# Kernel optimization log

Hardware: AMD Instinct MI355X
Metric: run time of the kernel (lower is better)

The kernel has to match this reference:

```python
import jax, jax.numpy as jnp
import numpy as np

X_MIN, X_MAX = -3.0, 3.0
EPS = 1e-08


def setup_inputs() -> dict:
    key = jax.random.key(0)
    k1, k2, k3 = jax.random.split(key, 3)
    B, D_in, D_out, K = 8192, 512, 128, 16
    x = jax.random.normal(k1, (B, D_in), dtype=jnp.float32)
    # trunc_normal_(std=0.02) approximated by scaled normal
    weights = jax.random.normal(k2, (D_out, D_in, K), dtype=jnp.float32) * 0.02
    # xavier_uniform for skip
    limit = float(np.sqrt(6.0 / (D_in + D_out)))
    skip_w = jax.random.uniform(k3, (D_out, D_in), dtype=jnp.float32,
                                minval=-limit, maxval=limit)
    bias = jnp.zeros((D_out,), dtype=jnp.float32)
    return {"x": x, "weights": weights, "skip_w": skip_w, "bias": bias}


def reference(x, weights, skip_w, bias):
    # x: (B, D_in); weights: (D_out, D_in, K); skip_w: (D_out, D_in); bias: (D_out,)
    K = weights.shape[-1]
    t = jnp.clip((x - X_MIN) / (X_MAX - X_MIN + EPS), 0.0, 1.0)
    pos = t * (K - 1)
    idx0 = jnp.floor(pos).astype(jnp.int32)
    idx1 = jnp.minimum(idx0 + 1, K - 1)
    frac = jnp.clip(pos - idx0.astype(pos.dtype), 0.0, 1.0)
    # Hat-basis coefficients per (b, i): avoids materializing (B, D_out, D_in)
    oh0 = jax.nn.one_hot(idx0, K, dtype=x.dtype)  # (B, D_in, K)
    oh1 = jax.nn.one_hot(idx1, K, dtype=x.dtype)
    c = oh0 * (1.0 - frac)[..., None] + oh1 * frac[..., None]  # (B, D_in, K)
    # y[b,o] = sum_i (1-frac)*w[o,i,idx0] + frac*w[o,i,idx1]
    y = jnp.einsum('bik,oik->bo', c, weights)
    y = y + bias + x @ skip_w.T
    return y
```

## Files before the change

kernel.cpp:

```cpp
#include <hip/hip_runtime.h>

typedef __attribute__((ext_vector_type(8))) short short8;
typedef __attribute__((ext_vector_type(4))) float f32x4;

#define DIN 512
#define DOUT 128
#define KK 16
#define BTOT 8192
#define KAUG (DIN * KK + DIN)
#define NCHUNK_TOT (KAUG / 128)
#define NSPL 4
#define CPB (NCHUNK_TOT / NSPL)
#define BM 64
#define CHUNK_BYTES 32768
#define CBASE 32768
#define LDS_BYTES 49152

__device__ static inline unsigned short f2bf(float x) {
  unsigned u = __builtin_bit_cast(unsigned, x);
  return (unsigned short)((u + 0x7FFFu + ((u >> 16) & 1u)) >> 16);
}

__device__ static inline void llds16(const char* g, char* l) {
  __builtin_amdgcn_global_load_lds(
      (const __attribute__((address_space(1))) unsigned int*)g,
      (__attribute__((address_space(3))) unsigned int*)l, 16, 0, 0);
}

__global__ __launch_bounds__(256) void build_wpp(const float* __restrict__ w,
                                                 const float* __restrict__ sk,
                                                 unsigned short* __restrict__ wpp) {
  const int gi = blockIdx.x * 256 + threadIdx.x;
  const int g = gi >> 11;
  const int rem = gi & 2047;
  const int o = rem >> 4;
  const int kcs = rem & 15;
  const int kc = kcs ^ (o & 15);
  const int kglob = g * 128 + kc * 8;
  const float* src = (kglob < 8192) ? (w + (size_t)o * 8192 + kglob)
                                    : (sk + (size_t)o * 512 + (kglob - 8192));
  const float4 v0 = ((const float4*)src)[0];
  const float4 v1 = ((const float4*)src)[1];
  uint4 pk;
  pk.x = f2bf(v0.x) | ((unsigned)f2bf(v0.y) << 16);
  pk.y = f2bf(v0.z) | ((unsigned)f2bf(v0.w) << 16);
  pk.z = f2bf(v1.x) | ((unsigned)f2bf(v1.y) << 16);
  pk.w = f2bf(v1.z) | ((unsigned)f2bf(v1.w) << 16);
  ((uint4*)wpp)[gi] = pk;
}

__global__ __launch_bounds__(256, 2) void kan_mfma(const float* __restrict__ x,
                                                   const unsigned short* __restrict__ wpp,
                                                   const float* __restrict__ bias,
                                                   float* __restrict__ out) {
  __shared__ __align__(16) char smem[LDS_BYTES];
  const int tid = threadIdx.x;
  const int bt = blockIdx.x >> 2;
  const int sp = blockIdx.x & 3;
  const int b0 = bt * BM;
  const int wid = tid >> 6, lane = tid & 63;
  const int lr = lane & 15, lq = lane >> 4;
  const int wm = wid & 1, wn = wid >> 1;

  f32x4 acc[2][4] = {};

  for (int c = 0; c < CPB; ++c) {
    const int g = sp * CPB + c;
    __syncthreads();

    {
      const char* gsrc = ((const char*)wpp) + (size_t)g * CHUNK_BYTES + wid * 8192 + lane * 16;
      char* ldst = smem + wid * 8192;
#pragma unroll
      for (int it = 0; it < 8; ++it)
        llds16(gsrc + it * 1024, ldst + it * 1024);
    }

    if (g < 64) {
      const int ibase = g * 8;
#pragma unroll
      for (int hh = 0; hh < 2; ++hh) {
        const int p = tid + hh * 256;
        const int bl = p >> 3, il = p & 7;
        const float xv = x[(size_t)(b0 + bl) * DIN + ibase + il];
        float t = fminf(fmaxf((xv + 3.0f) * (1.0f / 6.0f), 0.0f), 1.0f);
        const float pos = t * 15.0f;
        int i0 = (int)pos;
        i0 = i0 > 14 ? 14 : i0;
        const float f = pos - (float)i0;
        char* row = smem + CBASE + bl * 256;
        const int swz = bl & 15;
        char* g0 = row + (((il * 2) ^ swz) << 4);
        char* g1 = row + (((il * 2 + 1) ^ swz) << 4);
        *(uint4*)g0 = make_uint4(0, 0, 0, 0);
        *(uint4*)g1 = make_uint4(0, 0, 0, 0);
        const unsigned short h0 = f2bf(1.0f - f);
        const unsigned short h1 = f2bf(f);
        const int i1 = i0 + 1;
        *(unsigned short*)(((i0 & 8) ? g1 : g0) + (i0 & 7) * 2) = h0;
        *(unsigned short*)(((i1 & 8) ? g1 : g0) + (i1 & 7) * 2) = h1;
      }
    } else {
      const int ioff = (g - 64) * 128;
      const int bl = tid >> 2, q = tid & 3;
      const float* xr = x + (size_t)(b0 + bl) * DIN + ioff;
      char* row = smem + CBASE + bl * 256;
      const int swz = bl & 15;
#pragma unroll
      for (int gg = 0; gg < 4; ++gg) {
        const int kc = q * 4 + gg;
        const float4 v0 = ((const float4*)(xr + kc * 8))[0];
        const float4 v1 = ((const float4*)(xr + kc * 8))[1];
        uint4 pk;
        pk.x = f2bf(v0.x) | ((unsigned)f2bf(v0.y) << 16);
        pk.y = f2bf(v0.z) | ((unsigned)f2bf(v0.w) << 16);
        pk.z = f2bf(v1.x) | ((unsigned)f2bf(v1.y) << 16);
        pk.w = f2bf(v1.z) | ((unsigned)f2bf(v1.w) << 16);
        *(uint4*)(row + ((kc ^ swz) << 4)) = pk;
      }
    }
    __syncthreads();

#pragma unroll
    for (int ks = 0; ks < 4; ++ks) {
      const int swq = ((ks * 4 + lq) ^ lr) << 4;
      short8 af[2], bfr[4];
#pragma unroll
      for (int mt = 0; mt < 2; ++mt) {
        const int m = wm * 32 + mt * 16 + lr;
        af[mt] = *(const short8*)(smem + CBASE + m * 256 + swq);
      }
#pragma unroll
      for (int nt = 0; nt < 4; ++nt) {
        const int o = wn * 64 + nt * 16 + lr;
        bfr[nt] = *(const short8*)(smem + o * 256 + swq);
      }
#pragma unroll
      for (int mt = 0; mt < 2; ++mt)
#pragma unroll
        for (int nt = 0; nt < 4; ++nt)
          acc[mt][nt] = __builtin_amdgcn_mfma_f32_16x16x32_bf16(af[mt], bfr[nt], acc[mt][nt], 0, 0, 0);
    }
  }

#pragma unroll
  for (int nt = 0; nt < 4; ++nt) {
    const int col = wn * 64 + nt * 16 + lr;
    const float bv = (sp == 0) ? bias[col] : 0.0f;
#pragma unroll
    for (int mt = 0; mt < 2; ++mt) {
      const int rowb = b0 + wm * 32 + mt * 16 + lq * 4;
#pragma unroll
      for (int r = 0; r < 4; ++r)
        atomicAdd(out + (size_t)(rowb + r) * DOUT + col, acc[mt][nt][r] + bv);
    }
  }
}

__global__ void kan_naive(const float* __restrict__ x, const float* __restrict__ w,
                          const float* __restrict__ skw, const float* __restrict__ bias,
                          float* __restrict__ out) {
  const int b = blockIdx.x;
  const int o = threadIdx.x;
  float acc = bias[o];
  for (int i = 0; i < DIN; ++i) {
    float xv = x[(size_t)b * DIN + i];
    float t = fminf(fmaxf((xv + 3.0f) * (1.0f / 6.0f), 0.0f), 1.0f);
    float p = t * 15.0f;
    float fi = floorf(p);
    int i0 = (int)fi;
    int i1 = (i0 < 15) ? i0 + 1 : 15;
    float f = p - fi;
    const float* wr = &w[((size_t)o * DIN + i) * KK];
    acc += (1.0f - f) * wr[i0] + f * wr[i1] + xv * skw[(size_t)o * DIN + i];
  }
  out[(size_t)b * DOUT + o] = acc;
}

extern "C" void kernel_launch(void* const* d_in, const int* in_sizes, int n_in,
                              void* d_out, int out_size, void* d_ws, size_t ws_size,
                              hipStream_t stream) {
  const float* x    = (const float*)d_in[0];
  const float* w    = (const float*)d_in[1];
  const float* skw  = (const float*)d_in[2];
  const float* bias = (const float*)d_in[3];
  float* out = (float*)d_out;

  const size_t need = (size_t)NCHUNK_TOT * CHUNK_BYTES;
  if (ws_size < need) {
    kan_naive<<<BTOT, DOUT, 0, stream>>>(x, w, skw, bias, out);
    return;
  }

  unsigned short* wpp = (unsigned short*)d_ws;

  hipMemsetAsync(d_out, 0, (size_t)out_size * sizeof(float), stream);
  build_wpp<<<NCHUNK_TOT * 2048 / 256, 256, 0, stream>>>(w, skw, wpp);
  kan_mfma<<<(BTOT / BM) * NSPL, 256, 0, stream>>>(x, wpp, bias, out);
}
```

Before: 108.7 us.

## Double-buffer weight chunks and build spline A-fragments directly in registers

Weight chunks are now double-buffered in LDS, with the next chunk's async global-to-LDS load issued before the current chunk's MFMAs. This leaves one barrier per chunk instead of two. The hat-basis and skip A-operands are built per lane straight into MFMA fragment registers from prefetched x values, so the LDS staging, zeroing and readback of the coefficient tile go away. The cost is 64KB of LDS per block, which may limit occupancy at launch bounds 2, plus redundant spline computation across the waves that share rows.

```diff
diff --git a/kernel.cpp b/kernel.cpp
--- a/kernel.cpp
+++ b/kernel.cpp
@@ -2,6 +2,7 @@
 
 typedef __attribute__((ext_vector_type(8))) short short8;
 typedef __attribute__((ext_vector_type(4))) float f32x4;
+typedef __attribute__((ext_vector_type(4))) unsigned uint4v;
 
 #define DIN 512
 #define DOUT 128
@@ -13,8 +14,7 @@
 #define CPB (NCHUNK_TOT / NSPL)
 #define BM 64
 #define CHUNK_BYTES 32768
-#define CBASE 32768
-#define LDS_BYTES 49152
+#define LDS_BYTES 65536
 
 __device__ static inline unsigned short f2bf(float x) {
   unsigned u = __builtin_bit_cast(unsigned, x);
@@ -25,6 +25,34 @@
   __builtin_amdgcn_global_load_lds(
       (const __attribute__((address_space(1))) unsigned int*)g,
       (__attribute__((address_space(3))) unsigned int*)l, 16, 0, 0);
+}
+
+__device__ static inline short8 spline_granule(float xv, int half) {
+  float t = fminf(fmaxf((xv + 3.0f) * (1.0f / 6.0f), 0.0f), 1.0f);
+  float pos = t * 15.0f;
+  int i0 = (int)pos;
+  i0 = i0 > 14 ? 14 : i0;
+  float f = pos - (float)i0;
+  unsigned h0 = f2bf(1.0f - f);
+  unsigned h1 = f2bf(f);
+  unsigned long long P = (unsigned long long)(h0 | ((unsigned)h1 << 16));
+  const int j0 = i0 - (half << 3);
+  const unsigned ju = (unsigned)j0;
+  unsigned long long Pl = P << ((j0 & 3) << 4);
+  unsigned long long spill = P >> 16;
+  unsigned long long lo = (ju < 4u) ? Pl : ((j0 == -1) ? spill : 0ULL);
+  unsigned long long hi = ((ju - 4u) < 4u) ? Pl : ((j0 == 3) ? spill : 0ULL);
+  struct U { unsigned long long a, b; } u{lo, hi};
+  return __builtin_bit_cast(short8, u);
+}
+
+__device__ static inline short8 pack8(float4 a, float4 b) {
+  uint4v p;
+  p.x = f2bf(a.x) | ((unsigned)f2bf(a.y) << 16);
+  p.y = f2bf(a.z) | ((unsigned)f2bf(a.w) << 16);
+  p.z = f2bf(b.x) | ((unsigned)f2bf(b.y) << 16);
+  p.w = f2bf(b.z) | ((unsigned)f2bf(b.w) << 16);
+  return __builtin_bit_cast(short8, p);
 }
 
 __global__ __launch_bounds__(256) void build_wpp(const float* __restrict__ w,
@@ -61,86 +89,98 @@
   const int wid = tid >> 6, lane = tid & 63;
   const int lr = lane & 15, lq = lane >> 4;
   const int wm = wid & 1, wn = wid >> 1;
+  const int g0 = sp * CPB;
 
   f32x4 acc[2][4] = {};
 
-  for (int c = 0; c < CPB; ++c) {
-    const int g = sp * CPB + c;
-    __syncthreads();
-
-    {
-      const char* gsrc = ((const char*)wpp) + (size_t)g * CHUNK_BYTES + wid * 8192 + lane * 16;
-      char* ldst = smem + wid * 8192;
-#pragma unroll
-      for (int it = 0; it < 8; ++it)
-        llds16(gsrc + it * 1024, ldst + it * 1024);
-    }
-
+  const float* xr0 = x + (size_t)(b0 + wm * 32 + lr) * DIN;
+  const float* xr1 = xr0 + 16 * DIN;
+
+  {
+    const char* gsrc = (const char*)wpp + (size_t)g0 * CHUNK_BYTES + wid * 8192 + lane * 16;
+    char* ldst = smem + wid * 8192;
+#pragma unroll
+    for (int it = 0; it < 8; ++it) llds16(gsrc + it * 1024, ldst + it * 1024);
+  }
+  float xvA[2][4], xvB[2][4];
+  {
+    const int ib = g0 * 8 + (lq >> 1);
+#pragma unroll
+    for (int ks = 0; ks < 4; ++ks) {
+      xvA[0][ks] = xr0[ib + ks * 2];
+      xvA[1][ks] = xr1[ib + ks * 2];
+    }
+  }
+  __syncthreads();
+
+  auto chunk_body = [&](int c, int cb, float (&xcur)[2][4], float (&xnxt)[2][4]) {
+    const int g = g0 + c;
+    const bool haveNext = (c + 1 < CPB);
+
+    float4 r0[4][2], r1[4][2];
+    if (g >= 64) {
+      const int koff = (g - 64) * 128 + lq * 8;
+#pragma unroll
+      for (int ks = 0; ks < 4; ++ks) {
+        r0[ks][0] = ((const float4*)(xr0 + koff + ks * 32))[0];
+        r0[ks][1] = ((const float4*)(xr0 + koff + ks * 32))[1];
+        r1[ks][0] = ((const float4*)(xr1 + koff + ks * 32))[0];
+        r1[ks][1] = ((const float4*)(xr1 + koff + ks * 32))[1];
+      }
+    }
+
+    if (haveNext) {
+      const char* gsrc = (const char*)wpp + (size_t)(g + 1) * CHUNK_BYTES + wid * 8192 + lane * 16;
+      char* ldst = smem + (cb ^ 32768) + wid * 8192;
+#pragma unroll
+      for (int it = 0; it < 8; ++it) llds16(gsrc + it * 1024, ldst + it * 1024);
+    }
+    if (haveNext && (g + 1 < 64)) {
+      const int ib = (g + 1) * 8 + (lq >> 1);
+#pragma unroll
+      for (int ks = 0; ks < 4; ++ks) {
+        xnxt[0][ks] = xr0[ib + ks * 2];
+        xnxt[1][ks] = xr1[ib + ks * 2];
+      }
+    }
+
+    short8 af[2][4];
     if (g < 64) {
-      const int ibase = g * 8;
-#pragma unroll
-      for (int hh = 0; hh < 2; ++hh) {
-        const int p = tid + hh * 256;
-        const int bl = p >> 3, il = p & 7;
-        const float xv = x[(size_t)(b0 + bl) * DIN + ibase + il];
-        float t = fminf(fmaxf((xv + 3.0f) * (1.0f / 6.0f), 0.0f), 1.0f);
-        const float pos = t * 15.0f;
-        int i0 = (int)pos;
-        i0 = i0 > 14 ? 14 : i0;
-        const float f = pos - (float)i0;
-        char* row = smem + CBASE + bl * 256;
-        const int swz = bl & 15;
-        char* g0 = row + (((il * 2) ^ swz) << 4);
-        char* g1 = row + (((il * 2 + 1) ^ swz) << 4);
-        *(uint4*)g0 = make_uint4(0, 0, 0, 0);
-        *(uint4*)g1 = make_uint4(0, 0, 0, 0);
-        const unsigned short h0 = f2bf(1.0f - f);
-        const unsigned short h1 = f2bf(f);
-        const int i1 = i0 + 1;
-        *(unsigned short*)(((i0 & 8) ? g1 : g0) + (i0 & 7) * 2) = h0;
-        *(unsigned short*)(((i1 & 8) ? g1 : g0) + (i1 & 7) * 2) = h1;
+      const int half = lq & 1;
+#pragma unroll
+      for (int ks = 0; ks < 4; ++ks) {
+        af[0][ks] = spline_granule(xcur[0][ks], half);
+        af[1][ks] = spline_granule(xcur[1][ks], half);
       }
     } else {
-      const int ioff = (g - 64) * 128;
-      const int bl = tid >> 2, q = tid & 3;
-      const float* xr = x + (size_t)(b0 + bl) * DIN + ioff;
-      char* row = smem + CBASE + bl * 256;
-      const int swz = bl & 15;
-#pragma unroll
-      for (int gg = 0; gg < 4; ++gg) {
-        const int kc = q * 4 + gg;
-        const float4 v0 = ((const float4*)(xr + kc * 8))[0];
-        const float4 v1 = ((const float4*)(xr + kc * 8))[1];
-        uint4 pk;
-        pk.x = f2bf(v0.x) | ((unsigned)f2bf(v0.y) << 16);
-        pk.y = f2bf(v0.z) | ((unsigned)f2bf(v0.w) << 16);
-        pk.z = f2bf(v1.x) | ((unsigned)f2bf(v1.y) << 16);
-        pk.w = f2bf(v1.z) | ((unsigned)f2bf(v1.w) << 16);
-        *(uint4*)(row + ((kc ^ swz) << 4)) = pk;
-      }
-    }
-    __syncthreads();
+#pragma unroll
+      for (int ks = 0; ks < 4; ++ks) {
+        af[0][ks] = pack8(r0[ks][0], r0[ks][1]);
+        af[1][ks] = pack8(r1[ks][0], r1[ks][1]);
+      }
+    }
 
 #pragma unroll
     for (int ks = 0; ks < 4; ++ks) {
-      const int swq = ((ks * 4 + lq) ^ lr) << 4;
-      short8 af[2], bfr[4];
-#pragma unroll
-      for (int mt = 0; mt < 2; ++mt) {
-        const int m = wm * 32 + mt * 16 + lr;
-        af[mt] = *(const short8*)(smem + CBASE + m * 256 + swq);
-      }
+      const int gq = ((ks * 4 + lq) ^ lr) << 4;
+      short8 bfr[4];
 #pragma unroll
       for (int nt = 0; nt < 4; ++nt) {
         const int o = wn * 64 + nt * 16 + lr;
-        bfr[nt] = *(const short8*)(smem + o * 256 + swq);
+        bfr[nt] = *(const short8*)(smem + cb + o * 256 + gq);
       }
 #pragma unroll
       for (int mt = 0; mt < 2; ++mt)
 #pragma unroll
         for (int nt = 0; nt < 4; ++nt)
-          acc[mt][nt] = __builtin_amdgcn_mfma_f32_16x16x32_bf16(af[mt], bfr[nt], acc[mt][nt], 0, 0, 0);
-    }
+          acc[mt][nt] = __builtin_amdgcn_mfma_f32_16x16x32_bf16(af[mt][ks], bfr[nt], acc[mt][nt], 0, 0, 0);
+    }
+    __syncthreads();
+  };
+
+  for (int c = 0; c < CPB; c += 2) {
+    chunk_body(c, 0, xvA, xvB);
+    if (c + 1 < CPB) chunk_body(c + 1, 32768, xvB, xvA);
   }
 
 #pragma unroll
```

Measured after the change: 128.9 us. 1.19x slower.

## Double-buffer weight and coefficient tiles with larger 128-row blocks of 512 threads

Applied to the files above, without the earlier changes.

Doubles the batch tile to 128 rows and the block to 512 threads. Weight chunks and spline/skip coefficient tiles are now double-buffered in 128KB of dynamic LDS, so the next chunk's async global-to-LDS load and x load overlap the current MFMA work, leaving one barrier per iteration. Each weight chunk is now reused across twice as many rows. The cost is occupancy: 128KB of LDS per block likely allows only one block per CU, and the grid halves to 256 blocks, which may leave some of the 256 CUs idle.

```diff
diff --git a/kernel.cpp b/kernel.cpp
--- a/kernel.cpp
+++ b/kernel.cpp
@@ -11,10 +11,11 @@
 #define NCHUNK_TOT (KAUG / 128)
 #define NSPL 4
 #define CPB (NCHUNK_TOT / NSPL)
-#define BM 64
+#define BM 128
 #define CHUNK_BYTES 32768
-#define CBASE 32768
-#define LDS_BYTES 49152
+#define CT_BYTES 32768
+#define CBASE 65536
+#define LDS_BYTES 131072
 
 __device__ static inline unsigned short f2bf(float x) {
   unsigned u = __builtin_bit_cast(unsigned, x);
@@ -49,107 +50,132 @@
   ((uint4*)wpp)[gi] = pk;
 }
 
-__global__ __launch_bounds__(256, 2) void kan_mfma(const float* __restrict__ x,
+__global__ __launch_bounds__(512, 2) void kan_mfma(const float* __restrict__ x,
                                                    const unsigned short* __restrict__ wpp,
                                                    const float* __restrict__ bias,
                                                    float* __restrict__ out) {
-  __shared__ __align__(16) char smem[LDS_BYTES];
+  extern __shared__ __align__(16) char smem[];
   const int tid = threadIdx.x;
   const int bt = blockIdx.x >> 2;
   const int sp = blockIdx.x & 3;
   const int b0 = bt * BM;
   const int wid = tid >> 6, lane = tid & 63;
   const int lr = lane & 15, lq = lane >> 4;
-  const int wm = wid & 1, wn = wid >> 1;
-
-  f32x4 acc[2][4] = {};
+  const int wm = wid >> 2, wn = wid & 3;
+  const int g0 = sp * CPB;
+
+  f32x4 acc[4][2] = {};
+
+  auto stageW = [&](int g, int buf) {
+    const char* gsrc = ((const char*)wpp) + (size_t)g * CHUNK_BYTES + wid * 4096 + lane * 16;
+    char* ldst = smem + buf + wid * 4096;
+#pragma unroll
+    for (int it = 0; it < 4; ++it) llds16(gsrc + it * 1024, ldst + it * 1024);
+  };
+
+  auto buildSpline = [&](int cbuf, float xv0, float xv1) {
+#pragma unroll
+    for (int hh = 0; hh < 2; ++hh) {
+      const int p = tid + hh * 512;
+      const int bl = p >> 3, il = p & 7;
+      const float xv = hh ? xv1 : xv0;
+      float t = fminf(fmaxf((xv + 3.0f) * (1.0f / 6.0f), 0.0f), 1.0f);
+      const float pos = t * 15.0f;
+      int i0 = (int)pos;
+      i0 = i0 > 14 ? 14 : i0;
+      const float f = pos - (float)i0;
+      char* row = smem + cbuf + bl * 256;
+      const int swz = bl & 15;
+      char* gA = row + (((il * 2) ^ swz) << 4);
+      char* gB = row + (((il * 2 + 1) ^ swz) << 4);
+      *(uint4*)gA = make_uint4(0, 0, 0, 0);
+      *(uint4*)gB = make_uint4(0, 0, 0, 0);
+      const unsigned short h0 = f2bf(1.0f - f);
+      const unsigned short h1 = f2bf(f);
+      const int i1 = i0 + 1;
+      *(unsigned short*)(((i0 & 8) ? gB : gA) + (i0 & 7) * 2) = h0;
+      *(unsigned short*)(((i1 & 8) ? gB : gA) + (i1 & 7) * 2) = h1;
+    }
+  };
+
+  auto buildSkip = [&](int g, int cbuf) {
+    const int ioff = (g - 64) * 128;
+    const int bl = tid >> 2, q = tid & 3;
+    const float* xr = x + (size_t)(b0 + bl) * DIN + ioff;
+    char* row = smem + cbuf + bl * 256;
+    const int swz = bl & 15;
+#pragma unroll
+    for (int gg = 0; gg < 4; ++gg) {
+      const int kc = q * 4 + gg;
+      const float4 v0 = ((const float4*)(xr + kc * 8))[0];
+      const float4 v1 = ((const float4*)(xr + kc * 8))[1];
+      uint4 pk;
+      pk.x = f2bf(v0.x) | ((unsigned)f2bf(v0.y) << 16);
+      pk.y = f2bf(v0.z) | ((unsigned)f2bf(v0.w) << 16);
+      pk.z = f2bf(v1.x) | ((unsigned)f2bf(v1.y) << 16);
+      pk.w = f2bf(v1.z) | ((unsigned)f2bf(v1.w) << 16);
+      *(uint4*)(row + ((kc ^ swz) << 4)) = pk;
+    }
+  };
+
+  auto loadX = [&](int g, float& a, float& b) {
+    const int r0 = tid >> 3, il = tid & 7;
+    a = x[(size_t)(b0 + r0) * DIN + g * 8 + il];
+    b = x[(size_t)(b0 + 64 + r0) * DIN + g * 8 + il];
+  };
+
+  stageW(g0, 0);
+  {
+    float a, b;
+    loadX(g0, a, b);
+    buildSpline(CBASE + 0, a, b);
+  }
+  __syncthreads();
 
   for (int c = 0; c < CPB; ++c) {
-    const int g = sp * CPB + c;
-    __syncthreads();
-
-    {
-      const char* gsrc = ((const char*)wpp) + (size_t)g * CHUNK_BYTES + wid * 8192 + lane * 16;
-      char* ldst = smem + wid * 8192;
-#pragma unroll
-      for (int it = 0; it < 8; ++it)
-        llds16(gsrc + it * 1024, ldst + it * 1024);
-    }
-
-    if (g < 64) {
-      const int ibase = g * 8;
-#pragma unroll
-      for (int hh = 0; hh < 2; ++hh) {
-        const int p = tid + hh * 256;
-        const int bl = p >> 3, il = p & 7;
-        const float xv = x[(size_t)(b0 + bl) * DIN + ibase + il];
-        float t = fminf(fmaxf((xv + 3.0f) * (1.0f / 6.0f), 0.0f), 1.0f);
-        const float pos = t * 15.0f;
-        int i0 = (int)pos;
-        i0 = i0 > 14 ? 14 : i0;
-        const float f = pos - (float)i0;
-        char* row = smem + CBASE + bl * 256;
-        const int swz = bl & 15;
-        char* g0 = row + (((il * 2) ^ swz) << 4);
-        char* g1 = row + (((il * 2 + 1) ^ swz) << 4);
-        *(uint4*)g0 = make_uint4(0, 0, 0, 0);
-        *(uint4*)g1 = make_uint4(0, 0, 0, 0);
-        const unsigned short h0 = f2bf(1.0f - f);
-        const unsigned short h1 = f2bf(f);
-        const int i1 = i0 + 1;
-        *(unsigned short*)(((i0 & 8) ? g1 : g0) + (i0 & 7) * 2) = h0;
-        *(unsigned short*)(((i1 & 8) ? g1 : g0) + (i1 & 7) * 2) = h1;
-      }
-    } else {
-      const int ioff = (g - 64) * 128;
-      const int bl = tid >> 2, q = tid & 3;
-      const float* xr = x + (size_t)(b0 + bl) * DIN + ioff;
-      char* row = smem + CBASE + bl * 256;
-      const int swz = bl & 15;
-#pragma unroll
-      for (int gg = 0; gg < 4; ++gg) {
-        const int kc = q * 4 + gg;
-        const float4 v0 = ((const float4*)(xr + kc * 8))[0];
-        const float4 v1 = ((const float4*)(xr + kc * 8))[1];
-        uint4 pk;
-        pk.x = f2bf(v0.x) | ((unsigned)f2bf(v0.y) << 16);
-        pk.y = f2bf(v0.z) | ((unsigned)f2bf(v0.w) << 16);
-        pk.z = f2bf(v1.x) | ((unsigned)f2bf(v1.y) << 16);
-        pk.w = f2bf(v1.z) | ((unsigned)f2bf(v1.w) << 16);
-        *(uint4*)(row + ((kc ^ swz) << 4)) = pk;
-      }
-    }
-    __syncthreads();
-
+    const int g = g0 + c;
+    const int pb = (c & 1) << 15;
+    const int nb = pb ^ 32768;
+    const bool haveNext = (c + 1 < CPB);
+    const int gn = g + 1;
+
+    float xn0 = 0.0f, xn1 = 0.0f;
+    if (haveNext && gn < 64) loadX(gn, xn0, xn1);
+    if (haveNext) stageW(gn, nb);
+
+    const char* Wb = smem + pb;
+    const char* Cb = smem + CBASE + pb;
 #pragma unroll
     for (int ks = 0; ks < 4; ++ks) {
       const int swq = ((ks * 4 + lq) ^ lr) << 4;
-      short8 af[2], bfr[4];
-#pragma unroll
-      for (int mt = 0; mt < 2; ++mt) {
-        const int m = wm * 32 + mt * 16 + lr;
-        af[mt] = *(const short8*)(smem + CBASE + m * 256 + swq);
-      }
-#pragma unroll
-      for (int nt = 0; nt < 4; ++nt) {
-        const int o = wn * 64 + nt * 16 + lr;
-        bfr[nt] = *(const short8*)(smem + o * 256 + swq);
-      }
-#pragma unroll
-      for (int mt = 0; mt < 2; ++mt)
-#pragma unroll
-        for (int nt = 0; nt < 4; ++nt)
+      short8 af[4], bfr[2];
+#pragma unroll
+      for (int mt = 0; mt < 4; ++mt)
+        af[mt] = *(const short8*)(Cb + (wm * 64 + mt * 16 + lr) * 256 + swq);
+#pragma unroll
+      for (int nt = 0; nt < 2; ++nt)
+        bfr[nt] = *(const short8*)(Wb + (wn * 32 + nt * 16 + lr) * 256 + swq);
+#pragma unroll
+      for (int mt = 0; mt < 4; ++mt)
+#pragma unroll
+        for (int nt = 0; nt < 2; ++nt)
           acc[mt][nt] = __builtin_amdgcn_mfma_f32_16x16x32_bf16(af[mt], bfr[nt], acc[mt][nt], 0, 0, 0);
     }
-  }
-
-#pragma unroll
-  for (int nt = 0; nt < 4; ++nt) {
-    const int col = wn * 64 + nt * 16 + lr;
+
+    if (haveNext) {
+      if (gn < 64) buildSpline(CBASE + nb, xn0, xn1);
+      else buildSkip(gn, CBASE + nb);
+    }
+    __syncthreads();
+  }
+
+#pragma unroll
+  for (int nt = 0; nt < 2; ++nt) {
+    const int col = wn * 32 + nt * 16 + lr;
     const float bv = (sp == 0) ? bias[col] : 0.0f;
 #pragma unroll
-    for (int mt = 0; mt < 2; ++mt) {
-      const int rowb = b0 + wm * 32 + mt * 16 + lq * 4;
+    for (int mt = 0; mt < 4; ++mt) {
+      const int rowb = b0 + wm * 64 + mt * 16 + lq * 4;
 #pragma unroll
       for (int r = 0; r < 4; ++r)
         atomicAdd(out + (size_t)(rowb + r) * DOUT + col, acc[mt][nt][r] + bv);
@@ -186,8 +212,14 @@
   const float* bias = (const float*)d_in[3];
   float* out = (float*)d_out;
 
+  static bool lds_ok = []() {
+    return hipFuncSetAttribute((const void*)kan_mfma,
+                               hipFuncAttributeMaxDynamicSharedMemorySize,
+                               LDS_BYTES) == hipSuccess;
+  }();
+
   const size_t need = (size_t)NCHUNK_TOT * CHUNK_BYTES;
-  if (ws_size < need) {
+  if (ws_size < need || !lds_ok) {
     kan_naive<<<BTOT, DOUT, 0, stream>>>(x, w, skw, bias, out);
     return;
   }
@@ -196,5 +228,5 @@
 
   hipMemsetAsync(d_out, 0, (size_t)out_size * sizeof(float), stream);
   build_wpp<<<NCHUNK_TOT * 2048 / 256, 256, 0, stream>>>(w, skw, wpp);
-  kan_mfma<<<(BTOT / BM) * NSPL, 256, 0, stream>>>(x, wpp, bias, out);
-}
+  kan_mfma<<<(BTOT / BM) * NSPL, 512, LDS_BYTES, stream>>>(x, wpp, bias, out);
+}
```

Measured after the change: 110.2 us. About the same (+1.4%).

## Split K eight ways with partial buffers, reduce kernel, and x prefetch

Applied to the files above, without the earlier changes.

Raises the split-K factor from 4 to 8 with an uneven chunk assignment, so the 68 chunks are spread across twice as many blocks. Each split now writes its partial sums to a workspace slice, and a separate reduce kernel adds the slices and the bias, replacing the memset and the atomicAdd epilogue. The x values for the next spline chunk are prefetched into registers while the current chunk builds. The launch bound moves to 3 blocks per CU. The cost is 32 MB of partial-buffer traffic and an extra kernel launch, in exchange for more parallelism and no atomics.

```diff
diff --git a/kernel.cpp b/kernel.cpp
--- a/kernel.cpp
+++ b/kernel.cpp
@@ -8,13 +8,15 @@
 #define KK 16
 #define BTOT 8192
 #define KAUG (DIN * KK + DIN)
-#define NCHUNK_TOT (KAUG / 128)
-#define NSPL 4
-#define CPB (NCHUNK_TOT / NSPL)
+#define BK 128
+#define NCHUNK_TOT (KAUG / BK)
+#define NSPL 8
 #define BM 64
 #define CHUNK_BYTES 32768
 #define CBASE 32768
 #define LDS_BYTES 49152
+#define PART_OFF (4u << 20)
+#define OUT_ELEMS (BTOT * DOUT)
 
 __device__ static inline unsigned short f2bf(float x) {
   unsigned u = __builtin_bit_cast(unsigned, x);
@@ -49,78 +51,92 @@
   ((uint4*)wpp)[gi] = pk;
 }
 
-__global__ __launch_bounds__(256, 2) void kan_mfma(const float* __restrict__ x,
+__global__ __launch_bounds__(256, 3) void kan_mfma(const float* __restrict__ x,
                                                    const unsigned short* __restrict__ wpp,
-                                                   const float* __restrict__ bias,
-                                                   float* __restrict__ out) {
+                                                   float* __restrict__ part) {
   __shared__ __align__(16) char smem[LDS_BYTES];
   const int tid = threadIdx.x;
-  const int bt = blockIdx.x >> 2;
-  const int sp = blockIdx.x & 3;
+  const int bt = blockIdx.x >> 3;
+  const int sp = blockIdx.x & 7;
   const int b0 = bt * BM;
   const int wid = tid >> 6, lane = tid & 63;
   const int lr = lane & 15, lq = lane >> 4;
   const int wm = wid & 1, wn = wid >> 1;
+  const int g0 = sp * 8 + (sp < 4 ? sp : 4);
+  const int gend = g0 + (sp < 4 ? 9 : 8);
 
   f32x4 acc[2][4] = {};
 
-  for (int c = 0; c < CPB; ++c) {
-    const int g = sp * CPB + c;
-    __syncthreads();
-
-    {
-      const char* gsrc = ((const char*)wpp) + (size_t)g * CHUNK_BYTES + wid * 8192 + lane * 16;
-      char* ldst = smem + wid * 8192;
-#pragma unroll
-      for (int it = 0; it < 8; ++it)
-        llds16(gsrc + it * 1024, ldst + it * 1024);
-    }
-
-    if (g < 64) {
-      const int ibase = g * 8;
-#pragma unroll
-      for (int hh = 0; hh < 2; ++hh) {
-        const int p = tid + hh * 256;
-        const int bl = p >> 3, il = p & 7;
-        const float xv = x[(size_t)(b0 + bl) * DIN + ibase + il];
-        float t = fminf(fmaxf((xv + 3.0f) * (1.0f / 6.0f), 0.0f), 1.0f);
-        const float pos = t * 15.0f;
-        int i0 = (int)pos;
-        i0 = i0 > 14 ? 14 : i0;
-        const float f = pos - (float)i0;
-        char* row = smem + CBASE + bl * 256;
-        const int swz = bl & 15;
-        char* g0 = row + (((il * 2) ^ swz) << 4);
-        char* g1 = row + (((il * 2 + 1) ^ swz) << 4);
-        *(uint4*)g0 = make_uint4(0, 0, 0, 0);
-        *(uint4*)g1 = make_uint4(0, 0, 0, 0);
-        const unsigned short h0 = f2bf(1.0f - f);
-        const unsigned short h1 = f2bf(f);
-        const int i1 = i0 + 1;
-        *(unsigned short*)(((i0 & 8) ? g1 : g0) + (i0 & 7) * 2) = h0;
-        *(unsigned short*)(((i1 & 8) ? g1 : g0) + (i1 & 7) * 2) = h1;
-      }
-    } else {
-      const int ioff = (g - 64) * 128;
-      const int bl = tid >> 2, q = tid & 3;
-      const float* xr = x + (size_t)(b0 + bl) * DIN + ioff;
+  auto stageW = [&](int g) {
+    const char* gsrc = ((const char*)wpp) + (size_t)g * CHUNK_BYTES + wid * 8192 + lane * 16;
+    char* ldst = smem + wid * 8192;
+#pragma unroll
+    for (int it = 0; it < 8; ++it) llds16(gsrc + it * 1024, ldst + it * 1024);
+  };
+
+  auto loadX = [&](int g, float& a, float& b) {
+    const int r0 = tid >> 3, il = tid & 7;
+    a = x[(size_t)(b0 + r0) * DIN + g * 8 + il];
+    b = x[(size_t)(b0 + 32 + r0) * DIN + g * 8 + il];
+  };
+
+  auto buildSpline = [&](float xv0, float xv1) {
+#pragma unroll
+    for (int hh = 0; hh < 2; ++hh) {
+      const int bl = (tid >> 3) + hh * 32;
+      const int il = tid & 7;
+      const float xv = hh ? xv1 : xv0;
+      float t = fminf(fmaxf((xv + 3.0f) * (1.0f / 6.0f), 0.0f), 1.0f);
+      const float pos = t * 15.0f;
+      int i0 = (int)pos;
+      i0 = i0 > 14 ? 14 : i0;
+      const float f = pos - (float)i0;
       char* row = smem + CBASE + bl * 256;
       const int swz = bl & 15;
-#pragma unroll
-      for (int gg = 0; gg < 4; ++gg) {
-        const int kc = q * 4 + gg;
-        const float4 v0 = ((const float4*)(xr + kc * 8))[0];
-        const float4 v1 = ((const float4*)(xr + kc * 8))[1];
-        uint4 pk;
-        pk.x = f2bf(v0.x) | ((unsigned)f2bf(v0.y) << 16);
-        pk.y = f2bf(v0.z) | ((unsigned)f2bf(v0.w) << 16);
-        pk.z = f2bf(v1.x) | ((unsigned)f2bf(v1.y) << 16);
-        pk.w = f2bf(v1.z) | ((unsigned)f2bf(v1.w) << 16);
-        *(uint4*)(row + ((kc ^ swz) << 4)) = pk;
-      }
-    }
+      char* gA = row + (((il * 2) ^ swz) << 4);
+      char* gB = row + (((il * 2 + 1) ^ swz) << 4);
+      *(uint4*)gA = make_uint4(0, 0, 0, 0);
+      *(uint4*)gB = make_uint4(0, 0, 0, 0);
+      const unsigned short h0 = f2bf(1.0f - f);
+      const unsigned short h1 = f2bf(f);
+      const int i1 = i0 + 1;
+      *(unsigned short*)(((i0 & 8) ? gB : gA) + (i0 & 7) * 2) = h0;
+      *(unsigned short*)(((i1 & 8) ? gB : gA) + (i1 & 7) * 2) = h1;
+    }
+  };
+
+  auto buildSkip = [&](int g) {
+    const int ioff = (g - 64) * BK;
+    const int bl = tid >> 2, q = tid & 3;
+    const float* xr = x + (size_t)(b0 + bl) * DIN + ioff;
+    char* row = smem + CBASE + bl * 256;
+    const int swz = bl & 15;
+#pragma unroll
+    for (int gg = 0; gg < 4; ++gg) {
+      const int kc = q * 4 + gg;
+      const float4 v0 = ((const float4*)(xr + kc * 8))[0];
+      const float4 v1 = ((const float4*)(xr + kc * 8))[1];
+      uint4 pk;
+      pk.x = f2bf(v0.x) | ((unsigned)f2bf(v0.y) << 16);
+      pk.y = f2bf(v0.z) | ((unsigned)f2bf(v0.w) << 16);
+      pk.z = f2bf(v1.x) | ((unsigned)f2bf(v1.y) << 16);
+      pk.w = f2bf(v1.z) | ((unsigned)f2bf(v1.w) << 16);
+      *(uint4*)(row + ((kc ^ swz) << 4)) = pk;
+    }
+  };
+
+  float xa, xb;
+  loadX(g0, xa, xb);
+
+  for (int g = g0; g < gend; ++g) {
     __syncthreads();
-
+    stageW(g);
+    float na = 0.0f, nb = 0.0f;
+    const bool pf = (g + 1 < gend) && (g + 1 < 64);
+    if (pf) loadX(g + 1, na, nb);
+    if (g < 64) buildSpline(xa, xb);
+    else buildSkip(g);
+    __syncthreads();
 #pragma unroll
     for (int ks = 0; ks < 4; ++ks) {
       const int swq = ((ks * 4 + lq) ^ lr) << 4;
@@ -141,20 +157,36 @@
         for (int nt = 0; nt < 4; ++nt)
           acc[mt][nt] = __builtin_amdgcn_mfma_f32_16x16x32_bf16(af[mt], bfr[nt], acc[mt][nt], 0, 0, 0);
     }
-  }
-
+    if (pf) { xa = na; xb = nb; }
+  }
+
+  float* p = part + (size_t)sp * OUT_ELEMS;
 #pragma unroll
   for (int nt = 0; nt < 4; ++nt) {
     const int col = wn * 64 + nt * 16 + lr;
-    const float bv = (sp == 0) ? bias[col] : 0.0f;
 #pragma unroll
     for (int mt = 0; mt < 2; ++mt) {
       const int rowb = b0 + wm * 32 + mt * 16 + lq * 4;
 #pragma unroll
       for (int r = 0; r < 4; ++r)
-        atomicAdd(out + (size_t)(rowb + r) * DOUT + col, acc[mt][nt][r] + bv);
-    }
-  }
+        p[(size_t)(rowb + r) * DOUT + col] = acc[mt][nt][r];
+    }
+  }
+}
+
+__global__ __launch_bounds__(256) void kan_reduce(const float4* __restrict__ part,
+                                                  const float* __restrict__ bias,
+                                                  float4* __restrict__ out) {
+  const int id = blockIdx.x * 256 + threadIdx.x;
+  float4 s = part[id];
+#pragma unroll
+  for (int sp = 1; sp < NSPL; ++sp) {
+    const float4 v = part[(size_t)sp * (OUT_ELEMS / 4) + id];
+    s.x += v.x; s.y += v.y; s.z += v.z; s.w += v.w;
+  }
+  const float4 bv = ((const float4*)bias)[id & 31];
+  s.x += bv.x; s.y += bv.y; s.z += bv.z; s.w += bv.w;
+  out[id] = s;
 }
 
 __global__ void kan_naive(const float* __restrict__ x, const float* __restrict__ w,
@@ -186,15 +218,17 @@
   const float* bias = (const float*)d_in[3];
   float* out = (float*)d_out;
 
-  const size_t need = (size_t)NCHUNK_TOT * CHUNK_BYTES;
+  const size_t need = PART_OFF + (size_t)NSPL * OUT_ELEMS * sizeof(float);
   if (ws_size < need) {
     kan_naive<<<BTOT, DOUT, 0, stream>>>(x, w, skw, bias, out);
     return;
   }
 
   unsigned short* wpp = (unsigned short*)d_ws;
-
-  hipMemsetAsync(d_out, 0, (size_t)out_size * sizeof(float), stream);
+  float* part = (float*)((char*)d_ws + PART_OFF);
+
   build_wpp<<<NCHUNK_TOT * 2048 / 256, 256, 0, stream>>>(w, skw, wpp);
-  kan_mfma<<<(BTOT / BM) * NSPL, 256, 0, stream>>>(x, wpp, bias, out);
-}
+  kan_mfma<<<(BTOT / BM) * NSPL, 256, 0, stream>>>(x, wpp, part);
+  kan_reduce<<<OUT_ELEMS / 4 / 256, 256, 0, stream>>>((const float4*)part, bias,
+                                                      (float4*)out);
+}
```

Result: slower. 113.1 us (+4.1%).
